# Kernel tuning notes

Hardware: AMD Instinct MI355X
Metric: run time of the kernel (lower is better)

Reference implementation:

```python
import jax, jax.numpy as jnp
import numpy as np

EMBED_DIM = 64  # matches init_kwargs embed_dim; used for 1/sqrt(d) scaling


def setup_inputs() -> dict:
    key = jax.random.key(0)
    k1, k2, k3, k4 = jax.random.split(key, 4)
    N1, N2, C, B = 8192, 8192, EMBED_DIM, 8
    query = jax.random.normal(k1, (N1, C), dtype=jnp.float32)
    key_value = jax.random.normal(k2, (N2, C), dtype=jnp.float32)
    # sorted batch indices so per-batch concat order == input row order
    query_coors = jnp.sort(jax.random.randint(k3, (N1,), 0, B))
    key_value_coors = jnp.sort(jax.random.randint(k4, (N2,), 0, B))
    return {
        "query": query,
        "key_value": key_value,
        "query_coors": query_coors,
        "key_value_coors": key_value_coors,
    }


def reference(query, key_value, query_coors, key_value_coors):
    # Per-batch attention: each query row attends only to key_value rows with
    # the same batch index. Equivalent to the original per-batch loop +
    # chunked softmax(QK^T/sqrt(d)) V, expressed as one masked attention.
    # Dropout is identity (eval mode) for a deterministic correctness baseline.
    scale = 1.0 / jnp.sqrt(jnp.asarray(EMBED_DIM, dtype=query.dtype))
    scores = jnp.einsum("nc,mc->nm", query, key_value) * scale  # [N1, N2]
    same_batch = query_coors[:, None] == key_value_coors[None, :]
    neg_inf = jnp.asarray(-jnp.inf, dtype=scores.dtype)
    scores = jnp.where(same_batch, scores, neg_inf)
    attn = jax.nn.softmax(scores, axis=-1)  # softmax within each batch segment
    out = jnp.einsum("nm,mc->nc", attn, key_value)  # [N1, C]
    return out
```

## Files before the change

### kernel.cpp

```cpp
#include <hip/hip_runtime.h>
#include <hip/hip_bf16.h>

typedef __attribute__((ext_vector_type(8))) short bf16x8;
typedef __attribute__((ext_vector_type(8))) unsigned short u16x8;
typedef __attribute__((ext_vector_type(4))) float f32x4;

#define NEG_INF (-__builtin_inff())
#define SPLIT 4
#define QSCALE (0.125f * 1.4426950408889634f)
#define CONST_M 12.0f

static __device__ __forceinline__ unsigned short f2bf(float x) {
  union { float f; unsigned u; } v; v.f = x;
  unsigned r = (v.u + 0x7fffu + ((v.u >> 16) & 1u)) >> 16;
  return (unsigned short)r;
}

__global__ void prep_kv_kernel(const float* __restrict__ kv, const int* __restrict__ kvc,
                               unsigned short* __restrict__ kvb, unsigned short* __restrict__ kvt,
                               int* __restrict__ seg, int nkv) {
  __shared__ unsigned short tile[32][64];
  const int nb8 = gridDim.x >> 3;
  const int bp = ((gridDim.x & 7) == 0) ? ((blockIdx.x & 7) * nb8 + (blockIdx.x >> 3))
                                        : blockIdx.x;
  const int kv0 = bp * 32;
  const int t = threadIdx.x;
  if (t < 32) {
    int i = kv0 + t;
    if (i < nkv) {
      int c = kvc[i];
      int cp = (i == 0) ? -1 : kvc[i - 1];
      if (c != cp) {
        for (int b = cp + 1; b <= c; ++b) seg[b] = i;
        if (i == 0) for (int b = 0; b < c; ++b) seg[8 + b] = 0;
      }
      int cn = (i == nkv - 1) ? 8 : kvc[i + 1];
      if (c != cn) {
        for (int b = c; b < cn; ++b) seg[8 + b] = i + 1;
        if (i == nkv - 1) for (int b = c + 1; b < 8; ++b) seg[b] = nkv;
      }
    }
  }
  int r = (t * 8) >> 6;
  int c = (t * 8) & 63;
  const float4* src = (const float4*)(kv + (size_t)(kv0 + r) * 64 + c);
  float4 a = src[0], b = src[1];
  u16x8 v;
  v[0] = f2bf(a.x); v[1] = f2bf(a.y); v[2] = f2bf(a.z); v[3] = f2bf(a.w);
  v[4] = f2bf(b.x); v[5] = f2bf(b.y); v[6] = f2bf(b.z); v[7] = f2bf(b.w);
  *(u16x8*)&tile[r][c] = v;
  *(u16x8*)(kvb + (size_t)(kv0 + r) * 64 + c) = v;
  __syncthreads();
  int d = t & 63;
  int k0 = (t >> 6) * 8;
  u16x8 w;
#pragma unroll
  for (int j = 0; j < 8; ++j) w[j] = tile[k0 + j][d];
  *(u16x8*)(kvt + (size_t)bp * 2048 + d * 32 + k0) = w;
}

#define LOADK(P, kvx)                                                          \
  {                                                                            \
    const unsigned short* kb_ = kvb + (((size_t)((kvx) + rowoff)) << 6) + g8;  \
    k##P##0 = *(const bf16x8*)(kb_);                                           \
    k##P##1 = *(const bf16x8*)(kb_ + 32);                                      \
    k##P##2 = *(const bf16x8*)(kb_ + 256);                                     \
    k##P##3 = *(const bf16x8*)(kb_ + 256 + 32);                                \
  }

#define LOADV(P, kvx)                                                          \
  {                                                                            \
    const unsigned short* vb_ = kvt + (((size_t)(kvx) >> 5) << 11) + q16 * 32 + g8; \
    v##P##0 = *(const bf16x8*)(vb_);                                           \
    v##P##1 = *(const bf16x8*)(vb_ + 512);                                     \
    v##P##2 = *(const bf16x8*)(vb_ + 1024);                                    \
    v##P##3 = *(const bf16x8*)(vb_ + 1536);                                    \
  }

#define COMPUTE(P, kvx)                                                        \
  {                                                                            \
    const int kv0_ = (kvx);                                                    \
    f32x4 z_ = {0, 0, 0, 0};                                                   \
    __builtin_amdgcn_s_setprio(1);                                             \
    f32x4 sT0 = __builtin_amdgcn_mfma_f32_16x16x32_bf16(k##P##0, qf0, z_, 0, 0, 0); \
    sT0 = __builtin_amdgcn_mfma_f32_16x16x32_bf16(k##P##1, qf1, sT0, 0, 0, 0); \
    f32x4 sT1 = __builtin_amdgcn_mfma_f32_16x16x32_bf16(k##P##2, qf0, z_, 0, 0, 0); \
    sT1 = __builtin_amdgcn_mfma_f32_16x16x32_bf16(k##P##3, qf1, sT1, 0, 0, 0); \
    __builtin_amdgcn_s_setprio(0);                                             \
    float v_[8];                                                               \
    const bool full_ = uniformb && (kv0_ >= kv_lo) && (kv0_ + 32 <= kv_hi);    \
    if (full_) {                                                               \
      _Pragma("unroll") for (int r = 0; r < 4; ++r) {                          \
        v_[r] = sT0[r];                                                        \
        v_[4 + r] = sT1[r];                                                    \
      }                                                                        \
    } else {                                                                   \
      const int k0_ = kv0_ + g8;                                               \
      _Pragma("unroll") for (int r = 0; r < 4; ++r) {                          \
        v_[r]     = (k0_ + r     >= lo_q && k0_ + r     < hi_q) ? sT0[r] : NEG_INF; \
        v_[4 + r] = (k0_ + r + 4 >= lo_q && k0_ + r + 4 < hi_q) ? sT1[r] : NEG_INF; \
      }                                                                        \
    }                                                                          \
         \
    float t_ = fmaxf(fmaxf(fmaxf(v_[0], v_[1]), fmaxf(v_[2], v_[3])),          \
                     fmaxf(fmaxf(v_[4], v_[5]), fmaxf(v_[6], v_[7])));         \
    if (__builtin_expect(__any(t_ > m), 0)) {                                  \
      float tt_ = fmaxf(t_, __shfl_xor(t_, 16));                               \
      tt_ = fmaxf(tt_, __shfl_xor(tt_, 32));                                   \
      float mn_ = fmaxf(m, tt_);                                               \
      float f_ = __builtin_exp2f(m - mn_);                                     \
      l *= f_;                                                                 \
      _Pragma("unroll") for (int r = 0; r < 4; ++r) {                          \
        acc0[r] *= f_; acc1[r] *= f_; acc2[r] *= f_; acc3[r] *= f_;            \
      }                                                                        \
      m = mn_;                                                                 \
    }                                                                          \
    float e_[8];                                                               \
    _Pragma("unroll") for (int i = 0; i < 8; ++i)                              \
      e_[i] = __builtin_exp2f(v_[i] - m);          \
    l += (((e_[0] + e_[1]) + (e_[2] + e_[3])) +                                \
          ((e_[4] + e_[5]) + (e_[6] + e_[7])));                                \
    bf16x8 pa_;                                                                \
    _Pragma("unroll") for (int j = 0; j < 8; ++j) pa_[j] = (short)f2bf(e_[j]); \
    __builtin_amdgcn_s_setprio(1);                                             \
    acc0 = __builtin_amdgcn_mfma_f32_16x16x32_bf16(v##P##0, pa_, acc0, 0, 0, 0); \
    acc1 = __builtin_amdgcn_mfma_f32_16x16x32_bf16(v##P##1, pa_, acc1, 0, 0, 0); \
    acc2 = __builtin_amdgcn_mfma_f32_16x16x32_bf16(v##P##2, pa_, acc2, 0, 0, 0); \
    acc3 = __builtin_amdgcn_mfma_f32_16x16x32_bf16(v##P##3, pa_, acc3, 0, 0, 0); \
    __builtin_amdgcn_s_setprio(0);                                             \
  }

__global__ __launch_bounds__(256, 2) void attn_kernel(
    const float* __restrict__ qf,
    const unsigned short* __restrict__ kvb,
    const unsigned short* __restrict__ kvt,
    const int* __restrict__ qc,
    const int* __restrict__ seg,
    float* __restrict__ out, int n2)
{
  __shared__ float macc[SPLIT][16][68];
  __shared__ float mml[SPLIT][16];
  __shared__ float mll[SPLIT][16];

  const int nb8 = gridDim.x >> 3;
  const int bq = ((gridDim.x & 7) == 0) ? ((blockIdx.x & 7) * nb8 + (blockIdx.x >> 3))
                                        : blockIdx.x;
  const int q0 = bq * 16;
  const int w = threadIdx.x >> 6;
  const int lane = threadIdx.x & 63;
  const int q16 = lane & 15;
  const int g = lane >> 4;
  const int g8 = g * 8;

  const int myb = qc[q0 + q16];
  const int lo_q = seg[myb];
  const int hi_q = seg[8 + myb];
  const int bfirst = __shfl(myb, 0);
  const int blast  = __shfl(myb, 15);
  const int kv_lo  = __shfl(lo_q, 0);
  const int kv_hi  = __shfl(hi_q, 15);
  const bool uniformb = (bfirst == blast);

  bf16x8 qf0, qf1;
  {
    const float* qrow = qf + (size_t)(q0 + q16) * 64 + g8;
    float4 x0 = *(const float4*)(qrow);
    float4 x1 = *(const float4*)(qrow + 4);
    float4 x2 = *(const float4*)(qrow + 32);
    float4 x3 = *(const float4*)(qrow + 36);
    qf0[0]=(short)f2bf(x0.x*QSCALE); qf0[1]=(short)f2bf(x0.y*QSCALE);
    qf0[2]=(short)f2bf(x0.z*QSCALE); qf0[3]=(short)f2bf(x0.w*QSCALE);
    qf0[4]=(short)f2bf(x1.x*QSCALE); qf0[5]=(short)f2bf(x1.y*QSCALE);
    qf0[6]=(short)f2bf(x1.z*QSCALE); qf0[7]=(short)f2bf(x1.w*QSCALE);
    qf1[0]=(short)f2bf(x2.x*QSCALE); qf1[1]=(short)f2bf(x2.y*QSCALE);
    qf1[2]=(short)f2bf(x2.z*QSCALE); qf1[3]=(short)f2bf(x2.w*QSCALE);
    qf1[4]=(short)f2bf(x3.x*QSCALE); qf1[5]=(short)f2bf(x3.y*QSCALE);
    qf1[6]=(short)f2bf(x3.z*QSCALE); qf1[7]=(short)f2bf(x3.w*QSCALE);
  }

  const int base = kv_lo & ~31;
  const int nblk = (kv_hi - base + 31) >> 5;
  const int b0 = (nblk * w) / SPLIT;
  const int b1 = (nblk * (w + 1)) / SPLIT;

  const int rowoff = ((q16 >> 2) << 3) + (q16 & 3);

  f32x4 acc0 = {0,0,0,0}, acc1 = {0,0,0,0}, acc2 = {0,0,0,0}, acc3 = {0,0,0,0};
  float m = CONST_M;
  float l = 0.0f;

  bf16x8 kA0, kA1, kA2, kA3, kB0, kB1, kB2, kB3;
  bf16x8 vA0, vA1, vA2, vA3, vB0, vB1, vB2, vB3;
  int b = b0;
  if (b < b1) {
    LOADK(A, base + b * 32);
    LOADV(A, base + b * 32);
    while (true) {
      if (b + 1 < b1) { LOADK(B, base + (b + 1) * 32); LOADV(B, base + (b + 1) * 32); }
      COMPUTE(A, base + b * 32);
      ++b; if (b >= b1) break;
      if (b + 1 < b1) { LOADK(A, base + (b + 1) * 32); LOADV(A, base + (b + 1) * 32); }
      COMPUTE(B, base + b * 32);
      ++b; if (b >= b1) break;
    }
  }

  l += __shfl_xor(l, 16);
  l += __shfl_xor(l, 32);

#pragma unroll
  for (int r = 0; r < 4; ++r) {
    macc[w][q16][0  + g * 4 + r] = acc0[r];
    macc[w][q16][16 + g * 4 + r] = acc1[r];
    macc[w][q16][32 + g * 4 + r] = acc2[r];
    macc[w][q16][48 + g * 4 + r] = acc3[r];
  }
  if (g == 0) { mml[w][q16] = m; mll[w][q16] = l; }
  __syncthreads();

  {
    const int t = threadIdx.x;
    const int i = t >> 4;
    const int c0 = (t & 15) * 4;
    float mstar = NEG_INF;
#pragma unroll
    for (int ww = 0; ww < SPLIT; ++ww) mstar = fmaxf(mstar, mml[ww][i]);
    float s[SPLIT];
    float L = 0.0f;
#pragma unroll
    for (int ww = 0; ww < SPLIT; ++ww) {
      float mw = mml[ww][i];
      s[ww] = __builtin_exp2f(mw - mstar);
      L += s[ww] * mll[ww][i];
    }
    float inv = (L > 0.0f) ? 1.0f / L : 0.0f;
    f32x4 num = {0, 0, 0, 0};
#pragma unroll
    for (int ww = 0; ww < SPLIT; ++ww) {
      f32x4 a = *(const f32x4*)&macc[ww][i][c0];
      num[0] += s[ww] * a[0]; num[1] += s[ww] * a[1];
      num[2] += s[ww] * a[2]; num[3] += s[ww] * a[3];
    }
    float* o = out + (size_t)(q0 + i) * 64 + c0;
    o[0] = num[0] * inv; o[1] = num[1] * inv;
    o[2] = num[2] * inv; o[3] = num[3] * inv;
  }
}

extern "C" void kernel_launch(void* const* d_in, const int* in_sizes, int n_in,
                              void* d_out, int out_size, void* d_ws, size_t ws_size,
                              hipStream_t stream) {
  const float* q  = (const float*)d_in[0];
  const float* kv = (const float*)d_in[1];
  const int* qc   = (const int*)d_in[2];
  const int* kvc  = (const int*)d_in[3];
  float* out = (float*)d_out;

  const int C = 64;
  const int n1 = in_sizes[0] / C;
  const int n2 = in_sizes[1] / C;

  char* ws = (char*)d_ws;
  size_t off = 0;
  unsigned short* kvb = (unsigned short*)(ws + off); off += (size_t)n2 * C * 2;
  unsigned short* kvt = (unsigned short*)(ws + off); off += (size_t)n2 * C * 2;
  int* seg = (int*)(ws + off);

  prep_kv_kernel<<<n2 / 32, 256, 0, stream>>>(kv, kvc, kvb, kvt, seg, n2);
  attn_kernel<<<n1 / 16, 256, 0, stream>>>(q, kvb, kvt, qc, seg, out, n2);
}
```

Baseline: 30.63 us.

## Split KV range across blocks with global partials and separate merge kernel

```diff
diff --git a/kernel.cpp b/kernel.cpp
--- a/kernel.cpp
+++ b/kernel.cpp
@@ -2,11 +2,10 @@
 #include <hip/hip_bf16.h>
 
 typedef __attribute__((ext_vector_type(8))) short bf16x8;
-typedef __attribute__((ext_vector_type(8))) unsigned short u16x8;
+typedef __attribute__((ext_vector_type(4))) unsigned short u16x4;
 typedef __attribute__((ext_vector_type(4))) float f32x4;
 
 #define NEG_INF (-__builtin_inff())
-#define SPLIT 4
 #define QSCALE (0.125f * 1.4426950408889634f)
 #define CONST_M 12.0f
 
@@ -16,17 +15,18 @@
   return (unsigned short)r;
 }
 
-__global__ void prep_kv_kernel(const float* __restrict__ kv, const int* __restrict__ kvc,
-                               unsigned short* __restrict__ kvb, unsigned short* __restrict__ kvt,
-                               int* __restrict__ seg, int nkv) {
-  __shared__ unsigned short tile[32][64];
+__global__ __launch_bounds__(256) void prep_kv_kernel(
+    const float* __restrict__ kv, const int* __restrict__ kvc,
+    unsigned short* __restrict__ kvb, unsigned short* __restrict__ kvt,
+    int* __restrict__ seg, int nkv) {
+  __shared__ unsigned short tile[16][64];
   const int nb8 = gridDim.x >> 3;
   const int bp = ((gridDim.x & 7) == 0) ? ((blockIdx.x & 7) * nb8 + (blockIdx.x >> 3))
                                         : blockIdx.x;
-  const int kv0 = bp * 32;
+  const int rowbase = bp * 16;
   const int t = threadIdx.x;
-  if (t < 32) {
-    int i = kv0 + t;
+  if (t < 16) {
+    int i = rowbase + t;
     if (i < nkv) {
       int c = kvc[i];
       int cp = (i == 0) ? -1 : kvc[i - 1];
@@ -41,22 +41,22 @@
       }
     }
   }
-  int r = (t * 8) >> 6;
-  int c = (t * 8) & 63;
-  const float4* src = (const float4*)(kv + (size_t)(kv0 + r) * 64 + c);
-  float4 a = src[0], b = src[1];
-  u16x8 v;
-  v[0] = f2bf(a.x); v[1] = f2bf(a.y); v[2] = f2bf(a.z); v[3] = f2bf(a.w);
-  v[4] = f2bf(b.x); v[5] = f2bf(b.y); v[6] = f2bf(b.z); v[7] = f2bf(b.w);
-  *(u16x8*)&tile[r][c] = v;
-  *(u16x8*)(kvb + (size_t)(kv0 + r) * 64 + c) = v;
+  const int r = t >> 4;
+  const int c = (t & 15) * 4;
+  float4 a = *(const float4*)(kv + (size_t)(rowbase + r) * 64 + c);
+  u16x4 v4;
+  v4[0] = f2bf(a.x); v4[1] = f2bf(a.y); v4[2] = f2bf(a.z); v4[3] = f2bf(a.w);
+  *(u16x4*)(kvb + (size_t)(rowbase + r) * 64 + c) = v4;
+  *(u16x4*)&tile[r][c] = v4;
   __syncthreads();
-  int d = t & 63;
-  int k0 = (t >> 6) * 8;
-  u16x8 w;
-#pragma unroll
-  for (int j = 0; j < 8; ++j) w[j] = tile[k0 + j][d];
-  *(u16x8*)(kvt + (size_t)bp * 2048 + d * 32 + k0) = w;
+  const int d = t & 63;
+  const int k0 = (t >> 6) * 4;
+  u16x4 wv;
+#pragma unroll
+  for (int j = 0; j < 4; ++j) wv[j] = tile[k0 + j][d];
+  const int blk = rowbase >> 5;
+  const int kbase = (rowbase & 31) + k0;
+  *(u16x4*)(kvt + (size_t)blk * 2048 + d * 32 + kbase) = wv;
 }
 
 #define LOADK(P, kvx)                                                          \
@@ -101,7 +101,6 @@
         v_[4 + r] = (k0_ + r + 4 >= lo_q && k0_ + r + 4 < hi_q) ? sT1[r] : NEG_INF; \
       }                                                                        \
     }                                                                          \
-         \
     float t_ = fmaxf(fmaxf(fmaxf(v_[0], v_[1]), fmaxf(v_[2], v_[3])),          \
                      fmaxf(fmaxf(v_[4], v_[5]), fmaxf(v_[6], v_[7])));         \
     if (__builtin_expect(__any(t_ > m), 0)) {                                  \
@@ -136,23 +135,26 @@
     const unsigned short* __restrict__ kvt,
     const int* __restrict__ qc,
     const int* __restrict__ seg,
-    float* __restrict__ out, int n2)
+    float* __restrict__ pacc,
+    float2* __restrict__ pml,
+    int n2, int ncl2)
 {
-  __shared__ float macc[SPLIT][16][68];
-  __shared__ float mml[SPLIT][16];
-  __shared__ float mll[SPLIT][16];
-
-  const int nb8 = gridDim.x >> 3;
-  const int bq = ((gridDim.x & 7) == 0) ? ((blockIdx.x & 7) * nb8 + (blockIdx.x >> 3))
+  const int nc = 1 << ncl2;
+  const int per8 = gridDim.x >> 3;
+  const int ii = ((gridDim.x & 7) == 0) ? ((blockIdx.x & 7) * per8 + (blockIdx.x >> 3))
                                         : blockIdx.x;
-  const int q0 = bq * 16;
+  const int qt = ii >> ncl2;
+  const int c  = ii & (nc - 1);
+  const int qbase = qt * 64;
+
   const int w = threadIdx.x >> 6;
   const int lane = threadIdx.x & 63;
   const int q16 = lane & 15;
   const int g = lane >> 4;
   const int g8 = g * 8;
-
-  const int myb = qc[q0 + q16];
+  const int q0w = qbase + w * 16;
+
+  const int myb = qc[q0w + q16];
   const int lo_q = seg[myb];
   const int hi_q = seg[8 + myb];
   const int bfirst = __shfl(myb, 0);
@@ -163,7 +165,7 @@
 
   bf16x8 qf0, qf1;
   {
-    const float* qrow = qf + (size_t)(q0 + q16) * 64 + g8;
+    const float* qrow = qf + (size_t)(q0w + q16) * 64 + g8;
     float4 x0 = *(const float4*)(qrow);
     float4 x1 = *(const float4*)(qrow + 4);
     float4 x2 = *(const float4*)(qrow + 32);
@@ -180,8 +182,8 @@
 
   const int base = kv_lo & ~31;
   const int nblk = (kv_hi - base + 31) >> 5;
-  const int b0 = (nblk * w) / SPLIT;
-  const int b1 = (nblk * (w + 1)) / SPLIT;
+  const int b0 = (nblk * c) >> ncl2;
+  const int b1 = (nblk * (c + 1)) >> ncl2;
 
   const int rowoff = ((q16 >> 2) << 3) + (q16 & 3);
 
@@ -208,43 +210,58 @@
   l += __shfl_xor(l, 16);
   l += __shfl_xor(l, 32);
 
-#pragma unroll
-  for (int r = 0; r < 4; ++r) {
-    macc[w][q16][0  + g * 4 + r] = acc0[r];
-    macc[w][q16][16 + g * 4 + r] = acc1[r];
-    macc[w][q16][32 + g * 4 + r] = acc2[r];
-    macc[w][q16][48 + g * 4 + r] = acc3[r];
-  }
-  if (g == 0) { mml[w][q16] = m; mll[w][q16] = l; }
-  __syncthreads();
-
-  {
-    const int t = threadIdx.x;
-    const int i = t >> 4;
-    const int c0 = (t & 15) * 4;
-    float mstar = NEG_INF;
-#pragma unroll
-    for (int ww = 0; ww < SPLIT; ++ww) mstar = fmaxf(mstar, mml[ww][i]);
-    float s[SPLIT];
-    float L = 0.0f;
-#pragma unroll
-    for (int ww = 0; ww < SPLIT; ++ww) {
-      float mw = mml[ww][i];
-      s[ww] = __builtin_exp2f(mw - mstar);
-      L += s[ww] * mll[ww][i];
-    }
-    float inv = (L > 0.0f) ? 1.0f / L : 0.0f;
-    f32x4 num = {0, 0, 0, 0};
-#pragma unroll
-    for (int ww = 0; ww < SPLIT; ++ww) {
-      f32x4 a = *(const f32x4*)&macc[ww][i][c0];
-      num[0] += s[ww] * a[0]; num[1] += s[ww] * a[1];
-      num[2] += s[ww] * a[2]; num[3] += s[ww] * a[3];
-    }
-    float* o = out + (size_t)(q0 + i) * 64 + c0;
-    o[0] = num[0] * inv; o[1] = num[1] * inv;
-    o[2] = num[2] * inv; o[3] = num[3] * inv;
-  }
+  const int row = q0w + q16;
+  float* pr = pacc + ((size_t)row * nc + c) * 64;
+  *(f32x4*)(pr + 0  + g * 4) = acc0;
+  *(f32x4*)(pr + 16 + g * 4) = acc1;
+  *(f32x4*)(pr + 32 + g * 4) = acc2;
+  *(f32x4*)(pr + 48 + g * 4) = acc3;
+  if (g == 0) {
+    float2 v; v.x = m; v.y = l;
+    pml[(size_t)row * nc + c] = v;
+  }
+}
+
+__global__ __launch_bounds__(256) void merge_kernel(
+    const float* __restrict__ pacc, const float2* __restrict__ pml,
+    float* __restrict__ out, int ncl2)
+{
+  const int nc = 1 << ncl2;
+  const int nb8 = gridDim.x >> 3;
+  const int bq = ((gridDim.x & 7) == 0) ? ((blockIdx.x & 7) * nb8 + (blockIdx.x >> 3))
+                                        : blockIdx.x;
+  const int q0 = bq * 16;
+  const int t = threadIdx.x;
+  const int i = t >> 4;
+  const int c0 = (t & 15) * 4;
+  const int R = q0 + i;
+
+  float mm[4], ll[4], sc[4];
+  float mstar = NEG_INF;
+#pragma unroll
+  for (int cc = 0; cc < 4; ++cc) if (cc < nc) {
+    float2 v = pml[(size_t)R * nc + cc];
+    mm[cc] = v.x; ll[cc] = v.y;
+    mstar = fmaxf(mstar, v.x);
+  }
+  float L = 0.0f;
+#pragma unroll
+  for (int cc = 0; cc < 4; ++cc) if (cc < nc) {
+    sc[cc] = __builtin_exp2f(mm[cc] - mstar);
+    L += sc[cc] * ll[cc];
+  }
+  float inv = (L > 0.0f) ? 1.0f / L : 0.0f;
+  f32x4 num = {0, 0, 0, 0};
+#pragma unroll
+  for (int cc = 0; cc < 4; ++cc) if (cc < nc) {
+    f32x4 a = *(const f32x4*)&pacc[((size_t)R * nc + cc) * 64 + c0];
+    num[0] += sc[cc] * a[0]; num[1] += sc[cc] * a[1];
+    num[2] += sc[cc] * a[2]; num[3] += sc[cc] * a[3];
+  }
+  f32x4 o;
+  o[0] = num[0] * inv; o[1] = num[1] * inv;
+  o[2] = num[2] * inv; o[3] = num[3] * inv;
+  *(f32x4*)&out[(size_t)R * 64 + c0] = o;
 }
 
 extern "C" void kernel_launch(void* const* d_in, const int* in_sizes, int n_in,
@@ -260,12 +277,21 @@
   const int n1 = in_sizes[0] / C;
   const int n2 = in_sizes[1] / C;
 
+  const size_t fixed = (size_t)n2 * C * 2 * 2 + 4096;
+  int ncl2 = 0;
+  if (ws_size >= fixed + (size_t)n1 * 4 * (64 * 4 + 8)) ncl2 = 2;
+  else if (ws_size >= fixed + (size_t)n1 * 2 * (64 * 4 + 8)) ncl2 = 1;
+  const int nc = 1 << ncl2;
+
   char* ws = (char*)d_ws;
   size_t off = 0;
   unsigned short* kvb = (unsigned short*)(ws + off); off += (size_t)n2 * C * 2;
   unsigned short* kvt = (unsigned short*)(ws + off); off += (size_t)n2 * C * 2;
-  int* seg = (int*)(ws + off);
-
-  prep_kv_kernel<<<n2 / 32, 256, 0, stream>>>(kv, kvc, kvb, kvt, seg, n2);
-  attn_kernel<<<n1 / 16, 256, 0, stream>>>(q, kvb, kvt, qc, seg, out, n2);
-}
+  int* seg = (int*)(ws + off); off += 4096;
+  float* pacc = (float*)(ws + off); off += (size_t)n1 * nc * 64 * 4;
+  float2* pml = (float2*)(ws + off);
+
+  prep_kv_kernel<<<n2 / 16, 256, 0, stream>>>(kv, kvc, kvb, kvt, seg, n2);
+  attn_kernel<<<(n1 / 64) * nc, 256, 0, stream>>>(q, kvb, kvt, qc, seg, pacc, pml, n2, ncl2);
+  merge_kernel<<<n1 / 16, 256, 0, stream>>>(pacc, pml, out, ncl2);
+}
```

Measured after the change: 32.23 us. 1.05x slower.
